# Kernel optimization log

Measured on AMD Instinct MI355X. Metric: run time of the kernel, lower is better.

Reference implementation:

```python
import jax, jax.numpy as jnp
import numpy as np

N_NODES = 100_000
N_EDGES = 3_200_000
HIDDEN = 16


def setup_inputs() -> dict:
    key = jax.random.key(0)
    k1, k2, k3, k4 = jax.random.split(key, 4)
    x = jax.random.normal(k1, (N_NODES, 3), dtype=jnp.float32)
    edge_index = jax.random.randint(k2, (2, N_EDGES), 0, N_NODES, dtype=jnp.int32)
    # Glorot-style init for the two GCN layers (PyG GCNConv: lin weight + bias)
    W1 = jax.random.normal(k3, (3, HIDDEN), dtype=jnp.float32) * (1.0 / np.sqrt(3.0))
    b1 = jnp.zeros((HIDDEN,), dtype=jnp.float32)
    W2 = jax.random.normal(k4, (HIDDEN, 1), dtype=jnp.float32) * (1.0 / np.sqrt(HIDDEN))
    b2 = jnp.zeros((1,), dtype=jnp.float32)
    return {"x": x, "edge_index": edge_index, "W1": W1, "b1": b1, "W2": W2, "b2": b2}


def reference(x, edge_index, W1, b1, W2, b2):
    n = x.shape[0]  # static under jit
    # GCNConv default: add self-loops, symmetric degree normalization
    self_loop = jnp.arange(n, dtype=edge_index.dtype)
    src = jnp.concatenate([edge_index[0], self_loop])
    dst = jnp.concatenate([edge_index[1], self_loop])
    deg = jax.ops.segment_sum(jnp.ones_like(src, dtype=x.dtype), dst, num_segments=n)
    inv_sqrt_deg = jnp.where(deg > 0, jax.lax.rsqrt(jnp.maximum(deg, 1.0)), 0.0)
    norm = inv_sqrt_deg[src] * inv_sqrt_deg[dst]  # [E+N]

    def gcn_conv(h, W, b):
        h = h @ W  # linear transform first (cheaper: small out dim)
        msg = norm[:, None] * h[src]  # gather + scale
        return jax.ops.segment_sum(msg, dst, num_segments=n) + b  # scatter-add

    h = jax.nn.relu(gcn_conv(x, W1, b1))
    out = gcn_conv(h, W2, b2)
    return out.squeeze(-1)  # [N]
```

## Files before the change

### kernel.cpp

```cpp
#include <hip/hip_runtime.h>

#define HIDDEN 16
#define FB 128
#define FB_SHIFT 7
#define NBK_MAX 4096
#define FCHUNK 4096
#define FTH 512
#define SCAP 5120
#define NXCD 8
#define CB 1024
#define CB_SHIFT 10
#define NCB_MAX 512
#define CHUNK 4096
#define SPL 8
#define BT 1024

__device__ __forceinline__ int xcd_chunk(int bid, int nwg) {
    if (nwg < NXCD) return bid;
    int q = nwg / NXCD, r = nwg % NXCD;
    int x = bid % NXCD, k = bid / NXCD;
    return (x < r ? x * (q + 1) : r * (q + 1) + (x - r) * q) + k;
}


__global__ void k_zero(unsigned int* a, int na) {
    int i = blockIdx.x * blockDim.x + threadIdx.x;
    if (i < na) a[i] = 0u;
}

__global__ __launch_bounds__(FTH) void
k_histf(const int* __restrict__ dst, int e, int nbk, int nchunk,
        unsigned int* __restrict__ hcT) {
    __shared__ unsigned int h[NBK_MAX];
    for (int i = threadIdx.x; i < nbk; i += FTH) h[i] = 0u;
    __syncthreads();
    int c = xcd_chunk(blockIdx.x, nchunk);
    int start = c * FCHUNK;
    int end = min(start + FCHUNK, e);
    if (end - start == FCHUNK) {
        int i = start + threadIdx.x;
#pragma unroll
        for (int k = 0; k < FCHUNK / FTH; k++, i += FTH)
            atomicAdd(&h[((unsigned)dst[i]) >> FB_SHIFT], 1u);
    } else {
        for (int i = start + threadIdx.x; i < end; i += FTH)
            atomicAdd(&h[((unsigned)dst[i]) >> FB_SHIFT], 1u);
    }
    __syncthreads();
    for (int j = threadIdx.x; j < nbk; j += FTH)
        hcT[(size_t)j * nchunk + c] = h[j];
}

__global__ void k_scanf(unsigned int* __restrict__ hcT,
                        unsigned int* __restrict__ cntc, int nchunk) {
    __shared__ unsigned int ps[256];
    __shared__ unsigned int carry;
    int b = blockIdx.x, t = threadIdx.x;
    if (t == 0) carry = 0u;
    __syncthreads();
    size_t row = (size_t)b * nchunk;
    for (int t0 = 0; t0 < nchunk; t0 += 1024) {
        int i0 = t0 + t * 4;
        unsigned v0 = 0, v1 = 0, v2 = 0, v3 = 0;
        if (i0 + 3 < nchunk) {
            v0 = hcT[row + i0];     v1 = hcT[row + i0 + 1];
            v2 = hcT[row + i0 + 2]; v3 = hcT[row + i0 + 3];
        } else {
            if (i0     < nchunk) v0 = hcT[row + i0];
            if (i0 + 1 < nchunk) v1 = hcT[row + i0 + 1];
            if (i0 + 2 < nchunk) v2 = hcT[row + i0 + 2];
            if (i0 + 3 < nchunk) v3 = hcT[row + i0 + 3];
        }
        unsigned s1v = v0 + v1, s2v = s1v + v2, s3v = s2v + v3;
        ps[t] = s3v;
        __syncthreads();
        for (int off = 1; off < 256; off <<= 1) {
            unsigned u = (t >= off) ? ps[t - off] : 0u;
            __syncthreads();
            ps[t] += u;
            __syncthreads();
        }
        unsigned base = carry + ps[t] - s3v;
        if (i0     < nchunk) hcT[row + i0]     = base;
        if (i0 + 1 < nchunk) hcT[row + i0 + 1] = base + v0;
        if (i0 + 2 < nchunk) hcT[row + i0 + 2] = base + s1v;
        if (i0 + 3 < nchunk) hcT[row + i0 + 3] = base + s2v;
        __syncthreads();
        if (t == 255) carry += ps[255];
        __syncthreads();
    }
    if (t == 0) cntc[b] = carry;
}

__global__ __launch_bounds__(1024) void
k_scanb(const unsigned int* __restrict__ cntc, int nbk,
        unsigned int* __restrict__ basec,
        unsigned int* __restrict__ rowptr, int n, unsigned int e) {
    __shared__ unsigned int tsum[1024];
    int t = threadIdx.x;
    int K = (nbk + 1023) / 1024;
    unsigned int s = 0;
    for (int k = 0; k < K; k++) {
        int i = t * K + k;
        if (i < nbk) s += cntc[i];
    }
    tsum[t] = s;
    __syncthreads();
    for (int off = 1; off < 1024; off <<= 1) {
        unsigned int v = (t >= off) ? tsum[t - off] : 0u;
        __syncthreads();
        tsum[t] += v;
        __syncthreads();
    }
    unsigned int run = (t == 0) ? 0u : tsum[t - 1];
    for (int k = 0; k < K; k++) {
        int i = t * K + k;
        if (i < nbk) { basec[i] = run; run += cntc[i]; }
    }
    if (t == 1023) basec[nbk] = tsum[1023];
    if (t == 0) rowptr[n] = e;
}

__global__ __launch_bounds__(FTH) void
k_fillf(const int* __restrict__ src, const int* __restrict__ dst,
        int e, int nbk, int nchunk,
        const unsigned int* __restrict__ basec,
        const unsigned int* __restrict__ hcT,
        unsigned int* __restrict__ tmp) {
    __shared__ unsigned int h[NBK_MAX];
    __shared__ unsigned int lb[NBK_MAX];
    int c = xcd_chunk(blockIdx.x, nchunk);
    for (int j = threadIdx.x; j < nbk; j += FTH) {
        lb[j] = basec[j] + hcT[(size_t)j * nchunk + c];
        h[j] = 0u;
    }
    __syncthreads();
    int start = c * FCHUNK;
    int end = min(start + FCHUNK, e);
    if (end - start == FCHUNK) {
        int i = start + threadIdx.x;
#pragma unroll
        for (int k = 0; k < FCHUNK / FTH; k++, i += FTH) {
            unsigned int d = (unsigned)dst[i];
            unsigned int s = (unsigned)src[i];
            unsigned int b = d >> FB_SHIFT;
            unsigned int r = atomicAdd(&h[b], 1u);
            tmp[lb[b] + r] = (s << FB_SHIFT) | (d & (FB - 1u));
        }
    } else {
        for (int i = start + threadIdx.x; i < end; i += FTH) {
            unsigned int d = (unsigned)dst[i];
            unsigned int s = (unsigned)src[i];
            unsigned int b = d >> FB_SHIFT;
            unsigned int r = atomicAdd(&h[b], 1u);
            tmp[lb[b] + r] = (s << FB_SHIFT) | (d & (FB - 1u));
        }
    }
}

__global__ __launch_bounds__(FTH) void
k_cnt(const unsigned int* __restrict__ tmp,
      const unsigned int* __restrict__ basec,
      const float* __restrict__ x,
      unsigned int* __restrict__ rowptr, float4* __restrict__ xs4, int n) {
    __shared__ unsigned int cnt[FB];
    __shared__ unsigned int sc[FB];
    int t = threadIdx.x, b = blockIdx.x;
    unsigned int s = basec[b], endp = basec[b + 1];
    if (t < FB) cnt[t] = 0u;
    __syncthreads();
    unsigned int i = s + t;
    for (; i + 3u * FTH < endp; i += 4u * FTH) {
        unsigned r0 = tmp[i], r1 = tmp[i + FTH], r2 = tmp[i + 2u * FTH], r3 = tmp[i + 3u * FTH];
        atomicAdd(&cnt[r0 & (FB - 1u)], 1u);
        atomicAdd(&cnt[r1 & (FB - 1u)], 1u);
        atomicAdd(&cnt[r2 & (FB - 1u)], 1u);
        atomicAdd(&cnt[r3 & (FB - 1u)], 1u);
    }
    for (; i < endp; i += FTH)
        atomicAdd(&cnt[tmp[i] & (FB - 1u)], 1u);
    __syncthreads();
    if (t < FB) sc[t] = cnt[t];
    __syncthreads();
    for (int off = 1; off < FB; off <<= 1) {
        unsigned int v = (t < FB && t >= off) ? sc[t - off] : 0u;
        __syncthreads();
        if (t < FB && t >= off) sc[t] += v;
        __syncthreads();
    }
    if (t < FB) {
        int node = (b << FB_SHIFT) + t;
        if (node < n) {
            rowptr[node] = s + sc[t] - cnt[t];
            float iv = rsqrtf((float)(1u + cnt[t]));
            xs4[node] = make_float4(x[3 * node] * iv, x[3 * node + 1] * iv,
                                    x[3 * node + 2] * iv, iv);
        }
    }
}

__global__ __launch_bounds__(FTH) void
k_sortS1(const unsigned int* __restrict__ tmp,
         const unsigned int* __restrict__ basec,
         const unsigned int* __restrict__ rowptr,
         const float4* __restrict__ xs4,
         const float* __restrict__ W1, const float* __restrict__ b1,
         const float* __restrict__ W2, const float* __restrict__ b2,
         unsigned int* __restrict__ tmp2,
         float* __restrict__ t2s, float* __restrict__ out, int n) {
    __shared__ unsigned int lsort[SCAP];
    __shared__ unsigned int stn[FB];
    __shared__ unsigned int enn[FB];
    __shared__ unsigned int cur[FB];
    int t = threadIdx.x, b = blockIdx.x;
    unsigned int s = basec[b], endp = basec[b + 1], m = endp - s;
    if (t < FB) {
        int node = (b << FB_SHIFT) + t;
        unsigned int rp = (node < n) ? rowptr[node] : endp;
        unsigned int rq = (node < n) ? rowptr[node + 1] : endp;
        stn[t] = rp - s; enn[t] = rq - s; cur[t] = rp - s;
    }
    __syncthreads();
    bool fits = (m <= SCAP);
    if (fits) {
        unsigned int i = s + t;
        for (; i + 3u * FTH < endp; i += 4u * FTH) {
            unsigned r0 = tmp[i], r1 = tmp[i + FTH], r2 = tmp[i + 2u * FTH], r3 = tmp[i + 3u * FTH];
            unsigned p0 = atomicAdd(&cur[r0 & (FB - 1u)], 1u);
            unsigned p1 = atomicAdd(&cur[r1 & (FB - 1u)], 1u);
            unsigned p2 = atomicAdd(&cur[r2 & (FB - 1u)], 1u);
            unsigned p3 = atomicAdd(&cur[r3 & (FB - 1u)], 1u);
            lsort[p0] = r0 >> FB_SHIFT;
            lsort[p1] = r1 >> FB_SHIFT;
            lsort[p2] = r2 >> FB_SHIFT;
            lsort[p3] = r3 >> FB_SHIFT;
        }
        for (; i < endp; i += FTH) {
            unsigned rec = tmp[i];
            unsigned r = atomicAdd(&cur[rec & (FB - 1u)], 1u);
            lsort[r] = rec >> FB_SHIFT;
        }
        __syncthreads();
        for (unsigned int k = t; k < m; k += FTH)
            tmp2[s + k] = lsort[k];
    } else {
        for (unsigned int i = s + t; i < endp; i += FTH) {
            unsigned rec = tmp[i];
            unsigned r = atomicAdd(&cur[rec & (FB - 1u)], 1u);
            tmp2[s + r] = rec >> FB_SHIFT;
        }
        __syncthreads();
    }
    int nl = t >> 2, q = t & 3;
    int node = (b << FB_SHIFT) + nl;
    unsigned int st = stn[nl], en = enn[nl];
    float v0 = 0.f, v1 = 0.f, v2 = 0.f;
    if (fits) {
        for (unsigned int k = st + q; k < en; k += 4) {
            float4 p = xs4[lsort[k]];
            v0 += p.x; v1 += p.y; v2 += p.z;
        }
    } else {
        for (unsigned int k = st + q; k < en; k += 4) {
            float4 p = xs4[tmp2[s + k]];
            v0 += p.x; v1 += p.y; v2 += p.z;
        }
    }
    v0 += __shfl_xor(v0, 1); v0 += __shfl_xor(v0, 2);
    v1 += __shfl_xor(v1, 1); v1 += __shfl_xor(v1, 2);
    v2 += __shfl_xor(v2, 1); v2 += __shfl_xor(v2, 2);
    if (q == 0 && node < n) {
        float4 me = xs4[node];
        float iv = me.w;
        v0 = (v0 + me.x) * iv;
        v1 = (v1 + me.y) * iv;
        v2 = (v2 + me.z) * iv;
        float acc = 0.f;
#pragma unroll
        for (int k = 0; k < HIDDEN; k++) {
            float hh = fmaxf(fmaf(v0, W1[k], fmaf(v1, W1[HIDDEN + k],
                            fmaf(v2, W1[2 * HIDDEN + k], b1[k]))), 0.f);
            acc += hh * W2[k];
        }
        t2s[node] = acc * iv;
        out[node] = b2[0] + acc * iv * iv;
    }
}

__global__ void k_s2(const unsigned int* __restrict__ rowptr,
                     const unsigned int* __restrict__ tmp2,
                     const float* __restrict__ t2s, const float4* __restrict__ xs4,
                     float* __restrict__ out, int n) {
    int gid = blockIdx.x * blockDim.x + threadIdx.x;
    int i = gid >> 2, q = gid & 3;
    bool valid = (i < n);
    unsigned int s = 0, epos = 0;
    if (valid) { s = rowptr[i]; epos = rowptr[i + 1]; }
    float v = 0.f;
    unsigned int j = s + q;
    for (; j + 12 < epos; j += 16) {
        unsigned a0 = tmp2[j], a1 = tmp2[j + 4], a2 = tmp2[j + 8], a3 = tmp2[j + 12];
        v += (t2s[a0] + t2s[a1]) + (t2s[a2] + t2s[a3]);
    }
    for (; j < epos; j += 4) v += t2s[tmp2[j]];
    v += __shfl_xor(v, 1); v += __shfl_xor(v, 2);
    if (valid && q == 0) out[i] += v * xs4[i].w;
}


__global__ void k_hist_c(const int* __restrict__ dst, int e, int ncb, int nchunk,
                         unsigned int* __restrict__ cntc,
                         unsigned int* __restrict__ hcT) {
    __shared__ unsigned int h[NCB_MAX];
    for (int i = threadIdx.x; i < ncb; i += blockDim.x) h[i] = 0u;
    __syncthreads();
    int start = blockIdx.x * CHUNK;
    int end = min(start + CHUNK, e);
    for (int i = start + threadIdx.x; i < end; i += 256)
        atomicAdd(&h[((unsigned)dst[i]) >> CB_SHIFT], 1u);
    __syncthreads();
    for (int j = threadIdx.x; j < ncb; j += blockDim.x) {
        hcT[(size_t)j * nchunk + blockIdx.x] = h[j];
        if (h[j]) atomicAdd(&cntc[j], h[j]);
    }
}
__global__ void k_scan(const unsigned int* __restrict__ cnt, int nb,
                       unsigned int* __restrict__ base) {
    __shared__ unsigned int tsum[256];
    int t = threadIdx.x;
    int K = (nb + 255) / 256;
    unsigned int s = 0;
    for (int k = 0; k < K; k++) {
        int i = t * K + k;
        if (i < nb) s += cnt[i];
    }
    tsum[t] = s;
    __syncthreads();
    for (int off = 1; off < 256; off <<= 1) {
        unsigned int v = (t >= off) ? tsum[t - off] : 0u;
        __syncthreads();
        tsum[t] += v;
        __syncthreads();
    }
    unsigned int run = (t == 0) ? 0u : tsum[t - 1];
    for (int k = 0; k < K; k++) {
        int i = t * K + k;
        if (i < nb) { base[i] = run; run += cnt[i]; }
    }
}
__global__ void k_scanc(const unsigned int* __restrict__ hcT,
                        const unsigned int* __restrict__ basec,
                        unsigned int* __restrict__ lbasec, int nchunk) {
    __shared__ unsigned int ts[256];
    __shared__ unsigned int carry;
    int b = blockIdx.x, t = threadIdx.x;
    if (t == 0) carry = basec[b];
    __syncthreads();
    for (int t0 = 0; t0 < nchunk; t0 += 256) {
        int i = t0 + t;
        unsigned int v = (i < nchunk) ? hcT[(size_t)b * nchunk + i] : 0u;
        ts[t] = v;
        __syncthreads();
        for (int off = 1; off < 256; off <<= 1) {
            unsigned int u = (t >= off) ? ts[t - off] : 0u;
            __syncthreads();
            ts[t] += u;
            __syncthreads();
        }
        if (i < nchunk) lbasec[(size_t)b * nchunk + i] = carry + ts[t] - v;
        __syncthreads();
        if (t == 0) carry += ts[255];
        __syncthreads();
    }
}
__global__ void k_fill_c(const int* __restrict__ src, const int* __restrict__ dst,
                         int e, int ncb, int nchunk,
                         const unsigned int* __restrict__ lbasec,
                         unsigned int* __restrict__ tmp) {
    __shared__ unsigned int h[NCB_MAX];
    __shared__ unsigned int lb[NCB_MAX];
    for (int j = threadIdx.x; j < ncb; j += blockDim.x) {
        lb[j] = lbasec[(size_t)j * nchunk + blockIdx.x];
        h[j] = 0u;
    }
    __syncthreads();
    int start = blockIdx.x * CHUNK;
    int end = min(start + CHUNK, e);
    for (int i = start + threadIdx.x; i < end; i += 256) {
        unsigned int d = (unsigned)dst[i];
        unsigned int b = d >> CB_SHIFT;
        unsigned int r = atomicAdd(&h[b], 1u);
        tmp[lb[b] + r] = (((unsigned)src[i]) << CB_SHIFT) | (d & (CB - 1u));
    }
}
__global__ __launch_bounds__(BT) void
k_deg_split(const unsigned int* __restrict__ tmp, const unsigned int* __restrict__ basec,
            const unsigned int* __restrict__ cntc, unsigned int* __restrict__ deg, int n) {
    __shared__ unsigned int degl[CB];
    int t = threadIdx.x;
    degl[t] = 0u;
    __syncthreads();
    int b = blockIdx.x / SPL, sl = blockIdx.x % SPL;
    unsigned int s = basec[b], m = cntc[b];
    for (unsigned int i = sl * BT + t; i < m; i += SPL * BT)
        atomicAdd(&degl[tmp[s + i] & (CB - 1u)], 1u);
    __syncthreads();
    int node = b * CB + t;
    unsigned int c = degl[t];
    if (node < n && c) atomicAdd(&deg[node], c);
}
__global__ void k_inv_s(const unsigned int* __restrict__ deg, const float* __restrict__ x,
                        float4* __restrict__ xs4, int n) {
    int i = blockIdx.x * blockDim.x + threadIdx.x;
    if (i >= n) return;
    float iv = rsqrtf((float)(deg[i] + 1u));
    xs4[i] = make_float4(x[3 * i] * iv, x[3 * i + 1] * iv, x[3 * i + 2] * iv, iv);
}
__global__ __launch_bounds__(BT) void
k_s1_split(const unsigned int* __restrict__ tmp, const unsigned int* __restrict__ basec,
           const unsigned int* __restrict__ cntc, const float4* __restrict__ xs4,
           float* __restrict__ agg0, float* __restrict__ agg1, float* __restrict__ agg2, int n) {
    __shared__ float a0[CB], a1[CB], a2[CB];
    int t = threadIdx.x;
    a0[t] = 0.f; a1[t] = 0.f; a2[t] = 0.f;
    __syncthreads();
    int b = blockIdx.x / SPL, sl = blockIdx.x % SPL;
    unsigned int s = basec[b], m = cntc[b];
    for (unsigned int i = sl * BT + t; i < m; i += SPL * BT) {
        unsigned rec = tmp[s + i];
        float4 v = xs4[rec >> CB_SHIFT];
        unsigned dl = rec & (CB - 1u);
        atomicAdd(&a0[dl], v.x); atomicAdd(&a1[dl], v.y); atomicAdd(&a2[dl], v.z);
    }
    __syncthreads();
    int node = b * CB + t;
    if (node < n) {
        if (a0[t] != 0.f) atomicAdd(&agg0[node], a0[t]);
        if (a1[t] != 0.f) atomicAdd(&agg1[node], a1[t]);
        if (a2[t] != 0.f) atomicAdd(&agg2[node], a2[t]);
    }
}
__global__ void k_epi_s(const float* __restrict__ agg0, const float* __restrict__ agg1,
                        const float* __restrict__ agg2, const float4* __restrict__ xs4,
                        const float* __restrict__ W1, const float* __restrict__ b1,
                        const float* __restrict__ W2, const float* __restrict__ b2,
                        float* __restrict__ t2s, float* __restrict__ out, int n) {
    int i = blockIdx.x * blockDim.x + threadIdx.x;
    if (i >= n) return;
    float4 xv = xs4[i];
    float iv = xv.w;
    float v0 = iv * (agg0[i] + xv.x), v1 = iv * (agg1[i] + xv.y), v2 = iv * (agg2[i] + xv.z);
    float acc = 0.f;
#pragma unroll
    for (int j = 0; j < HIDDEN; j++) {
        float h = fmaxf(fmaf(v0, W1[j], fmaf(v1, W1[HIDDEN + j],
                       fmaf(v2, W1[2 * HIDDEN + j], b1[j]))), 0.f);
        acc += h * W2[j];
    }
    t2s[i] = acc * iv;
    out[i] = b2[0] + acc * iv * iv;
}
__global__ __launch_bounds__(BT) void
k_s2_split(const unsigned int* __restrict__ tmp, const unsigned int* __restrict__ basec,
           const unsigned int* __restrict__ cntc, const float* __restrict__ t2s,
           const float4* __restrict__ xs4, float* __restrict__ out, int n) {
    __shared__ float o[CB];
    int t = threadIdx.x;
    o[t] = 0.f;
    __syncthreads();
    int b = blockIdx.x / SPL, sl = blockIdx.x % SPL;
    unsigned int s = basec[b], m = cntc[b];
    for (unsigned int i = sl * BT + t; i < m; i += SPL * BT) {
        unsigned rec = tmp[s + i];
        atomicAdd(&o[rec & (CB - 1u)], t2s[rec >> CB_SHIFT]);
    }
    __syncthreads();
    int node = b * CB + t;
    if (node < n && o[t] != 0.f) atomicAdd(&out[node], o[t] * xs4[node].w);
}


extern "C" void kernel_launch(void* const* d_in, const int* in_sizes, int n_in,
                              void* d_out, int out_size, void* d_ws, size_t ws_size,
                              hipStream_t stream) {
    const float* x  = (const float*)d_in[0];
    const int*   ei = (const int*)d_in[1];
    const float* W1 = (const float*)d_in[2];
    const float* b1 = (const float*)d_in[3];
    const float* W2 = (const float*)d_in[4];
    const float* b2 = (const float*)d_in[5];
    float* out = (float*)d_out;

    int n = in_sizes[0] / 3;
    int e = in_sizes[1] / 2;
    const int* src = ei;
    const int* dst = ei + e;
    const int B = 256;

    int nbk = (n + FB - 1) / FB;
    int nchunkf = (e + FCHUNK - 1) / FCHUNK;
    int gridN4 = (4 * n + B - 1) / B;

    size_t needf = (size_t)n * 16 + (size_t)n * 4 + (size_t)(n + 1) * 4
                 + (size_t)(2 * nbk + 1) * 4 + (size_t)nbk * nchunkf * 4
                 + (size_t)e * 8 + 64;

    if (nbk <= NBK_MAX && n < (1 << 25) && ws_size >= needf) {
        float4* xs4 = (float4*)d_ws;
        float* t2s = (float*)(xs4 + n);
        unsigned int* rowptr = (unsigned int*)(t2s + n);
        unsigned int* cntc   = rowptr + (n + 1);
        unsigned int* basec  = cntc + nbk;
        unsigned int* hcT    = basec + nbk + 1;
        unsigned int* tmp    = hcT + (size_t)nbk * nchunkf;
        unsigned int* tmp2   = tmp + e;

        k_histf<<<nchunkf, FTH, 0, stream>>>(dst, e, nbk, nchunkf, hcT);
        k_scanf<<<nbk, 256, 0, stream>>>(hcT, cntc, nchunkf);
        k_scanb<<<1, 1024, 0, stream>>>(cntc, nbk, basec, rowptr, n, (unsigned)e);
        k_fillf<<<nchunkf, FTH, 0, stream>>>(src, dst, e, nbk, nchunkf, basec, hcT, tmp);
        k_cnt<<<nbk, FTH, 0, stream>>>(tmp, basec, x, rowptr, xs4, n);
        k_sortS1<<<nbk, FTH, 0, stream>>>(tmp, basec, rowptr, xs4, W1, b1, W2, b2,
                                          tmp2, t2s, out, n);
        k_s2<<<gridN4, B, 0, stream>>>(rowptr, tmp2, t2s, xs4, out, n);
    } else {
        int ncb = (n + CB - 1) / CB;
        int gridE = (e + CHUNK - 1) / CHUNK;
        int gridN = (n + B - 1) / B;
        float4* xs4 = (float4*)d_ws;
        float* agg0 = (float*)(xs4 + n);
        float* agg1 = agg0 + n;
        float* agg2 = agg1 + n;
        unsigned int* deg = (unsigned int*)(agg2 + n);
        float* t2s = (float*)(deg + n);
        unsigned int* cntc   = (unsigned int*)(t2s + n);
        unsigned int* basec  = cntc + ncb;
        unsigned int* hcT    = basec + ncb;
        unsigned int* lbasec = hcT + (size_t)ncb * gridE;
        unsigned int* tmp    = lbasec + (size_t)ncb * gridE;

        k_zero<<<(4 * n + ncb + B - 1) / B, B, 0, stream>>>((unsigned int*)agg0, 4 * n);
        k_zero<<<(ncb + B - 1) / B, B, 0, stream>>>(cntc, ncb);
        k_hist_c<<<gridE, B, 0, stream>>>(dst, e, ncb, gridE, cntc, hcT);
        k_scan<<<1, B, 0, stream>>>(cntc, ncb, basec);
        k_scanc<<<ncb, B, 0, stream>>>(hcT, basec, lbasec, gridE);
        k_fill_c<<<gridE, B, 0, stream>>>(src, dst, e, ncb, gridE, lbasec, tmp);
        k_deg_split<<<ncb * SPL, BT, 0, stream>>>(tmp, basec, cntc, deg, n);
        k_inv_s<<<gridN, B, 0, stream>>>(deg, x, xs4, n);
        k_s1_split<<<ncb * SPL, BT, 0, stream>>>(tmp, basec, cntc, xs4, agg0, agg1, agg2, n);
        k_epi_s<<<gridN, B, 0, stream>>>(agg0, agg1, agg2, xs4, W1, b1, W2, b2, t2s, out, n);
        k_s2_split<<<ncb * SPL, BT, 0, stream>>>(tmp, basec, cntc, t2s, xs4, out, n);
    }
}
```

Measured before the change: 159.0 us.

## Fuse count, sort, and both aggregation passes into one cooperative kernel

Replaces the k_cnt, k_sortS1 and k_s2 launches with a single cooperative kernel that uses grid-wide syncs between phases. Each block counts per-node degrees, computes normalized features, and locally sorts its bucket's source indices into LDS. It then does the first and second layer gathers straight from that LDS list instead of writing the sorted list to global memory and reading it back. This removes two kernel launch boundaries and a global round trip of the sorted edge array. In exchange it adds two grid syncs, uses 256 threads per block, and needs all blocks resident at once, which is why it only runs when nbk is at most 1024.

```diff
diff --git a/kernel.cpp b/kernel.cpp
--- a/kernel.cpp
+++ b/kernel.cpp
@@ -1,4 +1,7 @@
 #include <hip/hip_runtime.h>
+#include <hip/hip_cooperative_groups.h>
+
+namespace cg = cooperative_groups;
 
 #define HIDDEN 16
 #define FB 128
@@ -6,6 +9,7 @@
 #define NBK_MAX 4096
 #define FCHUNK 4096
 #define FTH 512
+#define MTH 256
 #define SCAP 5120
 #define NXCD 8
 #define CB 1024
@@ -157,6 +161,148 @@
         }
     }
 }
+
+__global__ __launch_bounds__(MTH, 4) void
+k_mega(const unsigned int* __restrict__ tmp,
+       const unsigned int* __restrict__ basec,
+       const float* __restrict__ x,
+       float4* __restrict__ xs4,
+       const float* __restrict__ W1, const float* __restrict__ b1,
+       const float* __restrict__ W2, const float* __restrict__ b2,
+       unsigned int* __restrict__ tmp2,
+       float* __restrict__ t2s, float* __restrict__ out, int n) {
+    cg::grid_group g = cg::this_grid();
+    __shared__ unsigned int lsort[SCAP];
+    __shared__ unsigned int stn[FB];
+    __shared__ unsigned int enn[FB];
+    __shared__ unsigned int cur[FB];
+    int t = threadIdx.x, b = blockIdx.x;
+    unsigned int s = basec[b], endp = basec[b + 1], m = endp - s;
+    if (t < FB) cur[t] = 0u;
+    __syncthreads();
+    {
+        unsigned int i = s + t;
+        for (; i + 3u * MTH < endp; i += 4u * MTH) {
+            unsigned r0 = tmp[i], r1 = tmp[i + MTH], r2 = tmp[i + 2u * MTH], r3 = tmp[i + 3u * MTH];
+            atomicAdd(&cur[r0 & (FB - 1u)], 1u);
+            atomicAdd(&cur[r1 & (FB - 1u)], 1u);
+            atomicAdd(&cur[r2 & (FB - 1u)], 1u);
+            atomicAdd(&cur[r3 & (FB - 1u)], 1u);
+        }
+        for (; i < endp; i += MTH)
+            atomicAdd(&cur[tmp[i] & (FB - 1u)], 1u);
+    }
+    __syncthreads();
+    if (t < FB) enn[t] = cur[t];
+    __syncthreads();
+    for (int off = 1; off < FB; off <<= 1) {
+        unsigned int v = (t < FB && t >= off) ? enn[t - off] : 0u;
+        __syncthreads();
+        if (t < FB && t >= off) enn[t] += v;
+        __syncthreads();
+    }
+    if (t < FB) {
+        unsigned int c = cur[t];
+        unsigned int st = enn[t] - c;
+        stn[t] = st;
+        cur[t] = st;
+        int node = (b << FB_SHIFT) + t;
+        if (node < n) {
+            float iv = rsqrtf((float)(1u + c));
+            xs4[node] = make_float4(x[3 * node] * iv, x[3 * node + 1] * iv,
+                                    x[3 * node + 2] * iv, iv);
+        }
+    }
+    g.sync();
+    bool fits = (m <= SCAP);
+    if (fits) {
+        unsigned int i = s + t;
+        for (; i + 3u * MTH < endp; i += 4u * MTH) {
+            unsigned r0 = tmp[i], r1 = tmp[i + MTH], r2 = tmp[i + 2u * MTH], r3 = tmp[i + 3u * MTH];
+            unsigned p0 = atomicAdd(&cur[r0 & (FB - 1u)], 1u);
+            unsigned p1 = atomicAdd(&cur[r1 & (FB - 1u)], 1u);
+            unsigned p2 = atomicAdd(&cur[r2 & (FB - 1u)], 1u);
+            unsigned p3 = atomicAdd(&cur[r3 & (FB - 1u)], 1u);
+            lsort[p0] = r0 >> FB_SHIFT;
+            lsort[p1] = r1 >> FB_SHIFT;
+            lsort[p2] = r2 >> FB_SHIFT;
+            lsort[p3] = r3 >> FB_SHIFT;
+        }
+        for (; i < endp; i += MTH) {
+            unsigned rec = tmp[i];
+            unsigned r = atomicAdd(&cur[rec & (FB - 1u)], 1u);
+            lsort[r] = rec >> FB_SHIFT;
+        }
+    } else {
+        for (unsigned int i = s + t; i < endp; i += MTH) {
+            unsigned rec = tmp[i];
+            unsigned r = atomicAdd(&cur[rec & (FB - 1u)], 1u);
+            tmp2[s + r] = rec >> FB_SHIFT;
+        }
+    }
+    __syncthreads();
+    int nl = t >> 1, q = t & 1;
+    int node = (b << FB_SHIFT) + nl;
+    unsigned int st = stn[nl], en = enn[nl];
+    float4 me = make_float4(0.f, 0.f, 0.f, 0.f);
+    if (node < n) me = xs4[node];
+    float v0 = 0.f, v1 = 0.f, v2 = 0.f;
+    {
+        unsigned int k = st + q;
+        if (fits) {
+            for (; k + 6 < en; k += 8) {
+                unsigned a0 = lsort[k], a1 = lsort[k + 2], a2 = lsort[k + 4], a3 = lsort[k + 6];
+                float4 p0 = xs4[a0], p1 = xs4[a1], p2 = xs4[a2], p3 = xs4[a3];
+                v0 += (p0.x + p1.x) + (p2.x + p3.x);
+                v1 += (p0.y + p1.y) + (p2.y + p3.y);
+                v2 += (p0.z + p1.z) + (p2.z + p3.z);
+            }
+            for (; k < en; k += 2) {
+                float4 p = xs4[lsort[k]];
+                v0 += p.x; v1 += p.y; v2 += p.z;
+            }
+        } else {
+            for (; k < en; k += 2) {
+                float4 p = xs4[tmp2[s + k]];
+                v0 += p.x; v1 += p.y; v2 += p.z;
+            }
+        }
+    }
+    v0 += __shfl_xor(v0, 1);
+    v1 += __shfl_xor(v1, 1);
+    v2 += __shfl_xor(v2, 1);
+    if (q == 0 && node < n) {
+        float iv = me.w;
+        float w0 = (v0 + me.x) * iv;
+        float w1 = (v1 + me.y) * iv;
+        float w2 = (v2 + me.z) * iv;
+        float acc = 0.f;
+#pragma unroll
+        for (int k = 0; k < HIDDEN; k++) {
+            float hh = fmaxf(fmaf(w0, W1[k], fmaf(w1, W1[HIDDEN + k],
+                            fmaf(w2, W1[2 * HIDDEN + k], b1[k]))), 0.f);
+            acc += hh * W2[k];
+        }
+        t2s[node] = acc * iv;
+        out[node] = b2[0] + acc * iv * iv;
+    }
+    g.sync();
+    float v = 0.f;
+    {
+        unsigned int k = st + q;
+        if (fits) {
+            for (; k + 6 < en; k += 8)
+                v += (t2s[lsort[k]] + t2s[lsort[k + 2]])
+                   + (t2s[lsort[k + 4]] + t2s[lsort[k + 6]]);
+            for (; k < en; k += 2) v += t2s[lsort[k]];
+        } else {
+            for (; k < en; k += 2) v += t2s[tmp2[s + k]];
+        }
+    }
+    v += __shfl_xor(v, 1);
+    if (q == 0 && node < n) out[node] += v * me.w;
+}
+
 
 __global__ __launch_bounds__(FTH) void
 k_cnt(const unsigned int* __restrict__ tmp,
@@ -519,10 +665,18 @@
         k_scanf<<<nbk, 256, 0, stream>>>(hcT, cntc, nchunkf);
         k_scanb<<<1, 1024, 0, stream>>>(cntc, nbk, basec, rowptr, n, (unsigned)e);
         k_fillf<<<nchunkf, FTH, 0, stream>>>(src, dst, e, nbk, nchunkf, basec, hcT, tmp);
-        k_cnt<<<nbk, FTH, 0, stream>>>(tmp, basec, x, rowptr, xs4, n);
-        k_sortS1<<<nbk, FTH, 0, stream>>>(tmp, basec, rowptr, xs4, W1, b1, W2, b2,
-                                          tmp2, t2s, out, n);
-        k_s2<<<gridN4, B, 0, stream>>>(rowptr, tmp2, t2s, xs4, out, n);
+        if (nbk <= 1024) {
+            void* args[] = {(void*)&tmp, (void*)&basec, (void*)&x, (void*)&xs4,
+                            (void*)&W1, (void*)&b1, (void*)&W2, (void*)&b2,
+                            (void*)&tmp2, (void*)&t2s, (void*)&out, (void*)&n};
+            hipLaunchCooperativeKernel((const void*)k_mega, dim3(nbk), dim3(MTH),
+                                       args, 0, stream);
+        } else {
+            k_cnt<<<nbk, FTH, 0, stream>>>(tmp, basec, x, rowptr, xs4, n);
+            k_sortS1<<<nbk, FTH, 0, stream>>>(tmp, basec, rowptr, xs4, W1, b1, W2, b2,
+                                              tmp2, t2s, out, n);
+            k_s2<<<gridN4, B, 0, stream>>>(rowptr, tmp2, t2s, xs4, out, n);
+        }
     } else {
         int ncb = (n + CB - 1) / CB;
         int gridE = (e + CHUNK - 1) / CHUNK;
```

After: 326.5 us. 105% more time.

## Record atomic ranks in a buffer to skip repeated shared atomics in fill and sort

Applied to the files above, without the earlier changes.

The histogram and count kernels now store each edge's rank from their shared-memory atomicAdd into a 16-bit global buffer. The fill and local-sort kernels read these ranks back instead of repeating the atomics, so the second pass no longer needs its own atomic counters. This trades LDS atomic contention for about 2 bytes per edge of extra global writes and reads, plus a larger workspace. Reusing the buffer between the two passes relies on the rank from histf being overwritten by k_cnt only after k_fillf has consumed it, which holds because the kernels run in order on the stream.

```diff
diff --git a/kernel.cpp b/kernel.cpp
--- a/kernel.cpp
+++ b/kernel.cpp
@@ -30,7 +30,7 @@
 
 __global__ __launch_bounds__(FTH) void
 k_histf(const int* __restrict__ dst, int e, int nbk, int nchunk,
-        unsigned int* __restrict__ hcT) {
+        unsigned int* __restrict__ hcT, unsigned short* __restrict__ rnk) {
     __shared__ unsigned int h[NBK_MAX];
     for (int i = threadIdx.x; i < nbk; i += FTH) h[i] = 0u;
     __syncthreads();
@@ -40,11 +40,15 @@
     if (end - start == FCHUNK) {
         int i = start + threadIdx.x;
 #pragma unroll
-        for (int k = 0; k < FCHUNK / FTH; k++, i += FTH)
-            atomicAdd(&h[((unsigned)dst[i]) >> FB_SHIFT], 1u);
+        for (int k = 0; k < FCHUNK / FTH; k++, i += FTH) {
+            unsigned int r = atomicAdd(&h[((unsigned)dst[i]) >> FB_SHIFT], 1u);
+            rnk[i] = (unsigned short)r;
+        }
     } else {
-        for (int i = start + threadIdx.x; i < end; i += FTH)
-            atomicAdd(&h[((unsigned)dst[i]) >> FB_SHIFT], 1u);
+        for (int i = start + threadIdx.x; i < end; i += FTH) {
+            unsigned int r = atomicAdd(&h[((unsigned)dst[i]) >> FB_SHIFT], 1u);
+            rnk[i] = (unsigned short)r;
+        }
     }
     __syncthreads();
     for (int j = threadIdx.x; j < nbk; j += FTH)
@@ -126,14 +130,12 @@
         int e, int nbk, int nchunk,
         const unsigned int* __restrict__ basec,
         const unsigned int* __restrict__ hcT,
+        const unsigned short* __restrict__ rnk,
         unsigned int* __restrict__ tmp) {
-    __shared__ unsigned int h[NBK_MAX];
     __shared__ unsigned int lb[NBK_MAX];
     int c = xcd_chunk(blockIdx.x, nchunk);
-    for (int j = threadIdx.x; j < nbk; j += FTH) {
+    for (int j = threadIdx.x; j < nbk; j += FTH)
         lb[j] = basec[j] + hcT[(size_t)j * nchunk + c];
-        h[j] = 0u;
-    }
     __syncthreads();
     int start = c * FCHUNK;
     int end = min(start + FCHUNK, e);
@@ -144,16 +146,14 @@
             unsigned int d = (unsigned)dst[i];
             unsigned int s = (unsigned)src[i];
             unsigned int b = d >> FB_SHIFT;
-            unsigned int r = atomicAdd(&h[b], 1u);
-            tmp[lb[b] + r] = (s << FB_SHIFT) | (d & (FB - 1u));
+            tmp[lb[b] + rnk[i]] = (s << FB_SHIFT) | (d & (FB - 1u));
         }
     } else {
         for (int i = start + threadIdx.x; i < end; i += FTH) {
             unsigned int d = (unsigned)dst[i];
             unsigned int s = (unsigned)src[i];
             unsigned int b = d >> FB_SHIFT;
-            unsigned int r = atomicAdd(&h[b], 1u);
-            tmp[lb[b] + r] = (s << FB_SHIFT) | (d & (FB - 1u));
+            tmp[lb[b] + rnk[i]] = (s << FB_SHIFT) | (d & (FB - 1u));
         }
     }
 }
@@ -162,7 +162,8 @@
 k_cnt(const unsigned int* __restrict__ tmp,
       const unsigned int* __restrict__ basec,
       const float* __restrict__ x,
-      unsigned int* __restrict__ rowptr, float4* __restrict__ xs4, int n) {
+      unsigned int* __restrict__ rowptr, float4* __restrict__ xs4,
+      unsigned short* __restrict__ rnk, int n) {
     __shared__ unsigned int cnt[FB];
     __shared__ unsigned int sc[FB];
     int t = threadIdx.x, b = blockIdx.x;
@@ -172,13 +173,19 @@
     unsigned int i = s + t;
     for (; i + 3u * FTH < endp; i += 4u * FTH) {
         unsigned r0 = tmp[i], r1 = tmp[i + FTH], r2 = tmp[i + 2u * FTH], r3 = tmp[i + 3u * FTH];
-        atomicAdd(&cnt[r0 & (FB - 1u)], 1u);
-        atomicAdd(&cnt[r1 & (FB - 1u)], 1u);
-        atomicAdd(&cnt[r2 & (FB - 1u)], 1u);
-        atomicAdd(&cnt[r3 & (FB - 1u)], 1u);
-    }
-    for (; i < endp; i += FTH)
-        atomicAdd(&cnt[tmp[i] & (FB - 1u)], 1u);
+        unsigned c0 = atomicAdd(&cnt[r0 & (FB - 1u)], 1u);
+        unsigned c1 = atomicAdd(&cnt[r1 & (FB - 1u)], 1u);
+        unsigned c2 = atomicAdd(&cnt[r2 & (FB - 1u)], 1u);
+        unsigned c3 = atomicAdd(&cnt[r3 & (FB - 1u)], 1u);
+        rnk[i]            = (unsigned short)c0;
+        rnk[i + FTH]      = (unsigned short)c1;
+        rnk[i + 2u * FTH] = (unsigned short)c2;
+        rnk[i + 3u * FTH] = (unsigned short)c3;
+    }
+    for (; i < endp; i += FTH) {
+        unsigned c0 = atomicAdd(&cnt[tmp[i] & (FB - 1u)], 1u);
+        rnk[i] = (unsigned short)c0;
+    }
     __syncthreads();
     if (t < FB) sc[t] = cnt[t];
     __syncthreads();
@@ -203,6 +210,7 @@
 k_sortS1(const unsigned int* __restrict__ tmp,
          const unsigned int* __restrict__ basec,
          const unsigned int* __restrict__ rowptr,
+         const unsigned short* __restrict__ rnk,
          const float4* __restrict__ xs4,
          const float* __restrict__ W1, const float* __restrict__ b1,
          const float* __restrict__ W2, const float* __restrict__ b2,
@@ -211,14 +219,13 @@
     __shared__ unsigned int lsort[SCAP];
     __shared__ unsigned int stn[FB];
     __shared__ unsigned int enn[FB];
-    __shared__ unsigned int cur[FB];
     int t = threadIdx.x, b = blockIdx.x;
     unsigned int s = basec[b], endp = basec[b + 1], m = endp - s;
     if (t < FB) {
         int node = (b << FB_SHIFT) + t;
         unsigned int rp = (node < n) ? rowptr[node] : endp;
         unsigned int rq = (node < n) ? rowptr[node + 1] : endp;
-        stn[t] = rp - s; enn[t] = rq - s; cur[t] = rp - s;
+        stn[t] = rp - s; enn[t] = rq - s;
     }
     __syncthreads();
     bool fits = (m <= SCAP);
@@ -226,19 +233,15 @@
         unsigned int i = s + t;
         for (; i + 3u * FTH < endp; i += 4u * FTH) {
             unsigned r0 = tmp[i], r1 = tmp[i + FTH], r2 = tmp[i + 2u * FTH], r3 = tmp[i + 3u * FTH];
-            unsigned p0 = atomicAdd(&cur[r0 & (FB - 1u)], 1u);
-            unsigned p1 = atomicAdd(&cur[r1 & (FB - 1u)], 1u);
-            unsigned p2 = atomicAdd(&cur[r2 & (FB - 1u)], 1u);
-            unsigned p3 = atomicAdd(&cur[r3 & (FB - 1u)], 1u);
-            lsort[p0] = r0 >> FB_SHIFT;
-            lsort[p1] = r1 >> FB_SHIFT;
-            lsort[p2] = r2 >> FB_SHIFT;
-            lsort[p3] = r3 >> FB_SHIFT;
+            unsigned k0 = rnk[i], k1 = rnk[i + FTH], k2 = rnk[i + 2u * FTH], k3 = rnk[i + 3u * FTH];
+            lsort[stn[r0 & (FB - 1u)] + k0] = r0 >> FB_SHIFT;
+            lsort[stn[r1 & (FB - 1u)] + k1] = r1 >> FB_SHIFT;
+            lsort[stn[r2 & (FB - 1u)] + k2] = r2 >> FB_SHIFT;
+            lsort[stn[r3 & (FB - 1u)] + k3] = r3 >> FB_SHIFT;
         }
         for (; i < endp; i += FTH) {
             unsigned rec = tmp[i];
-            unsigned r = atomicAdd(&cur[rec & (FB - 1u)], 1u);
-            lsort[r] = rec >> FB_SHIFT;
+            lsort[stn[rec & (FB - 1u)] + rnk[i]] = rec >> FB_SHIFT;
         }
         __syncthreads();
         for (unsigned int k = t; k < m; k += FTH)
@@ -246,8 +249,7 @@
     } else {
         for (unsigned int i = s + t; i < endp; i += FTH) {
             unsigned rec = tmp[i];
-            unsigned r = atomicAdd(&cur[rec & (FB - 1u)], 1u);
-            tmp2[s + r] = rec >> FB_SHIFT;
+            tmp2[s + stn[rec & (FB - 1u)] + rnk[i]] = rec >> FB_SHIFT;
         }
         __syncthreads();
     }
@@ -503,7 +505,7 @@
 
     size_t needf = (size_t)n * 16 + (size_t)n * 4 + (size_t)(n + 1) * 4
                  + (size_t)(2 * nbk + 1) * 4 + (size_t)nbk * nchunkf * 4
-                 + (size_t)e * 8 + 64;
+                 + (size_t)e * 8 + (size_t)e * 2 + 64;
 
     if (nbk <= NBK_MAX && n < (1 << 25) && ws_size >= needf) {
         float4* xs4 = (float4*)d_ws;
@@ -514,13 +516,14 @@
         unsigned int* hcT    = basec + nbk + 1;
         unsigned int* tmp    = hcT + (size_t)nbk * nchunkf;
         unsigned int* tmp2   = tmp + e;
-
-        k_histf<<<nchunkf, FTH, 0, stream>>>(dst, e, nbk, nchunkf, hcT);
+        unsigned short* rnk  = (unsigned short*)(tmp2 + e);
+
+        k_histf<<<nchunkf, FTH, 0, stream>>>(dst, e, nbk, nchunkf, hcT, rnk);
         k_scanf<<<nbk, 256, 0, stream>>>(hcT, cntc, nchunkf);
         k_scanb<<<1, 1024, 0, stream>>>(cntc, nbk, basec, rowptr, n, (unsigned)e);
-        k_fillf<<<nchunkf, FTH, 0, stream>>>(src, dst, e, nbk, nchunkf, basec, hcT, tmp);
-        k_cnt<<<nbk, FTH, 0, stream>>>(tmp, basec, x, rowptr, xs4, n);
-        k_sortS1<<<nbk, FTH, 0, stream>>>(tmp, basec, rowptr, xs4, W1, b1, W2, b2,
+        k_fillf<<<nchunkf, FTH, 0, stream>>>(src, dst, e, nbk, nchunkf, basec, hcT, rnk, tmp);
+        k_cnt<<<nbk, FTH, 0, stream>>>(tmp, basec, x, rowptr, xs4, rnk, n);
+        k_sortS1<<<nbk, FTH, 0, stream>>>(tmp, basec, rowptr, rnk, xs4, W1, b1, W2, b2,
                                           tmp2, t2s, out, n);
         k_s2<<<gridN4, B, 0, stream>>>(rowptr, tmp2, t2s, xs4, out, n);
     } else {
```

Result: slower. 162.5 us (+2.2%).
